# Kernel optimization log

Measured on AMD Instinct MI355X. Metric: run time of the kernel, lower is better.

## Reference

```python
import jax, jax.numpy as jnp
import numpy as np

# ---- static config (mirrors TALoss(num_classes=80, reg_max=16, strides=[8,16,32])) ----
B, M, NC, REG_MAX = 32, 20, 80, 16
STRIDES = (8, 16, 32)
HW = ((80, 80), (40, 40), (20, 20))          # feature map sizes for 640x640 input
NO = REG_MAX * 4 + NC                         # 144 channels per head
A = sum(h * w for h, w in HW)                 # 8400 anchors
TOPK, ALPHA, BETA = 10, 0.5, 6.0
BOX_G, CLS_G, DFL_G = 7.5, 0.5, 1.5
EPS = 1e-9


def setup_inputs() -> dict:
    key = jax.random.key(0)
    ks = jax.random.split(key, 6)
    feats = {f"feat{i}": jax.random.normal(ks[i], (B, NO, h, w), jnp.float32)
             for i, (h, w) in enumerate(HW)}
    # targets: (N,6) rows of (img_idx, class, cx, cy, w, h), normalized, 20 boxes/image, sorted by image
    img_idx = jnp.repeat(jnp.arange(B, dtype=jnp.float32), M)
    cls = jax.random.randint(ks[3], (B * M,), 0, NC).astype(jnp.float32)
    cxy = jax.random.uniform(ks[4], (B * M, 2), minval=0.2, maxval=0.8)
    wh = jax.random.uniform(ks[5], (B * M, 2), minval=0.05, maxval=0.3)
    targets = jnp.concatenate([img_idx[:, None], cls[:, None], cxy, wh], axis=1)
    return {**feats, "targets": targets}


def _make_anchors():
    pts, strs = [], []
    for (h, w), s in zip(HW, STRIDES):
        sx = jnp.arange(w, dtype=jnp.float32) + 0.5
        sy = jnp.arange(h, dtype=jnp.float32) + 0.5
        gy, gx = jnp.meshgrid(sy, sx, indexing="ij")
        pts.append(jnp.stack([gx, gy], -1).reshape(-1, 2))
        strs.append(jnp.full((h * w, 1), float(s), jnp.float32))
    return jnp.concatenate(pts), jnp.concatenate(strs)   # (A,2), (A,1)


def _ciou(b1, b2, eps=1e-7):
    # b1, b2: broadcastable xyxy boxes (..., 4) -> CIoU (...,)
    b1x1, b1y1, b1x2, b1y2 = b1[..., 0], b1[..., 1], b1[..., 2], b1[..., 3]
    b2x1, b2y1, b2x2, b2y2 = b2[..., 0], b2[..., 1], b2[..., 2], b2[..., 3]
    w1, h1 = b1x2 - b1x1, b1y2 - b1y1 + eps
    w2, h2 = b2x2 - b2x1, b2y2 - b2y1 + eps
    inter = (jnp.clip(jnp.minimum(b1x2, b2x2) - jnp.maximum(b1x1, b2x1), 0)
             * jnp.clip(jnp.minimum(b1y2, b2y2) - jnp.maximum(b1y1, b2y1), 0))
    union = w1 * h1 + w2 * h2 - inter + eps
    iou = inter / union
    cw = jnp.maximum(b1x2, b2x2) - jnp.minimum(b1x1, b2x1)
    ch = jnp.maximum(b1y2, b2y2) - jnp.minimum(b1y1, b2y1)
    c2 = cw ** 2 + ch ** 2 + eps
    rho2 = ((b2x1 + b2x2 - b1x1 - b1x2) ** 2 + (b2y1 + b2y2 - b1y1 - b1y2) ** 2) / 4.0
    v = (4.0 / np.pi ** 2) * (jnp.arctan(w2 / h2) - jnp.arctan(w1 / h1)) ** 2
    a = jax.lax.stop_gradient(v / (v - iou + (1.0 + eps)))   # torch: computed under no_grad
    return iou - (rho2 / c2 + v * a)


def _assign(pd_scores, pd_bboxes, anc, gt_labels, gt_bboxes, mask_gt):
    """TaskAlignedAssigner. pd_scores (B,A,NC) sigmoid-ed, pd_bboxes (B,A,4) image units,
    anc (A,2) image units, gt_labels (B,M), gt_bboxes (B,M,4), mask_gt (B,M) float."""
    # anchors inside each gt box -> (B,M,A)
    lt = anc[None, None, :, :] - gt_bboxes[:, :, None, :2]
    rb = gt_bboxes[:, :, None, 2:] - anc[None, None, :, :]
    mask_in = (jnp.concatenate([lt, rb], -1).min(-1) > EPS).astype(jnp.float32)
    mask = mask_in * mask_gt[..., None]                      # (B,M,A) candidate mask
    overlaps = jnp.clip(_ciou(gt_bboxes[:, :, None, :], pd_bboxes[:, None, :, :]), 0) * mask
    labels = gt_labels.astype(jnp.int32)                     # (B,M)
    # scores of each gt's class at every anchor: (B,M,A)
    bbox_scores = jnp.take_along_axis(pd_scores.transpose(0, 2, 1),
                                      jnp.broadcast_to(labels[:, :, None], (B, M, A)), axis=1) * mask
    align = (bbox_scores ** ALPHA) * (overlaps ** BETA)      # (B,M,A), already zero off-mask
    # top-k anchors per gt
    _, idxs = jax.lax.top_k(align, TOPK)                     # (B,M,K)
    idxs = jnp.where(mask_gt[..., None] > 0, idxs, 0)
    cnt = jax.nn.one_hot(idxs, A, dtype=jnp.float32).sum(-2)  # (B,M,A)
    mask_topk = jnp.where(cnt > 1, 0.0, cnt)
    mask_pos = mask_topk * mask
    # resolve anchors matched to multiple gts: keep the max-overlap gt
    fg = mask_pos.sum(1)                                     # (B,A)
    is_max = jnp.moveaxis(jax.nn.one_hot(overlaps.argmax(1), M, dtype=jnp.float32), -1, 1)  # (B,M,A)
    mask_pos = jnp.where(fg[:, None, :] > 1, is_max, mask_pos)
    fg = mask_pos.sum(1)
    tgt_idx = mask_pos.argmax(1)                             # (B,A)
    t_labels = jnp.take_along_axis(labels, tgt_idx, 1)       # (B,A)
    t_bboxes = jnp.take_along_axis(gt_bboxes, tgt_idx[..., None], 1)  # (B,A,4)
    fg_b = (fg > 0).astype(jnp.float32)
    t_scores = jax.nn.one_hot(t_labels, NC, dtype=jnp.float32) * fg_b[..., None]
    # normalize scores: align * (max overlap per gt) / (max align per gt)
    align_pos = align * mask_pos
    pos_align = align_pos.max(-1, keepdims=True)             # (B,M,1)
    pos_over = (overlaps * mask_pos).max(-1, keepdims=True)
    norm = (align_pos * pos_over / (pos_align + EPS)).max(1)  # (B,A)
    return t_bboxes, t_scores * norm[..., None], fg_b


def _forward(feat0, feat1, feat2, targets):
    feats = [feat0, feat1, feat2]
    pred = jnp.concatenate([f.reshape(B, NO, -1) for f in feats], axis=2)
    pred_distri = pred[:, :REG_MAX * 4].transpose(0, 2, 1)   # (B,A,64)
    pred_scores = pred[:, REG_MAX * 4:].transpose(0, 2, 1)   # (B,A,NC)
    anc, stride_t = _make_anchors()
    img_h, img_w = HW[0][0] * STRIDES[0], HW[0][1] * STRIDES[0]
    scale = jnp.array([img_w, img_h, img_w, img_h], jnp.float32)
    # ---- preprocess targets (N,6) -> padded (B,M,5), xywh*scale -> xyxy ----
    idx = targets[:, 0].astype(jnp.int32)
    pos = jnp.arange(targets.shape[0]) - jnp.searchsorted(idx, idx, side="left")
    out = jnp.zeros((B, M, 5), jnp.float32).at[idx, pos].set(targets[:, 1:])
    gt_labels = out[..., 0]
    xywh = out[..., 1:5] * scale
    gt_bboxes = jnp.concatenate([xywh[..., :2] - xywh[..., 2:] / 2,
                                 xywh[..., :2] + xywh[..., 2:] / 2], -1)
    mask_gt = (gt_bboxes.sum(-1) > 0).astype(jnp.float32)    # (B,M)
    # ---- DFL bbox decode (feature-map units) ----
    proj = jnp.arange(REG_MAX, dtype=jnp.float32)
    dist = jax.nn.softmax(pred_distri.reshape(B, A, 4, REG_MAX), -1) @ proj  # (B,A,4) ltrb
    pred_bboxes = jnp.concatenate([anc - dist[..., :2], anc + dist[..., 2:]], -1)
    # ---- task-aligned assignment (on detached preds, image units) ----
    pd_scores = jax.lax.stop_gradient(jax.nn.sigmoid(pred_scores))
    pd_bboxes = jax.lax.stop_gradient(pred_bboxes) * stride_t
    target_bboxes, target_scores, fg_mask = _assign(pd_scores, pd_bboxes, anc * stride_t,
                                                    gt_labels, gt_bboxes, mask_gt)
    target_bboxes = target_bboxes / stride_t
    tss = jnp.maximum(target_scores.sum(), 1.0)
    # ---- BCE-with-logits classification loss (pos_weight=1) ----
    x, t = pred_scores, target_scores
    bce = jnp.maximum(x, 0) - x * t + jnp.log1p(jnp.exp(-jnp.abs(x)))
    loss_cls = bce.sum() / tss
    # ---- CIoU box loss + DFL, weighted by per-anchor target score sum on fg ----
    weight = target_scores.sum(-1) * fg_mask                 # (B,A)
    iou = _ciou(pred_bboxes, target_bboxes)
    loss_box = ((1.0 - iou) * weight).sum() / tss
    tltrb = jnp.clip(jnp.concatenate([anc - target_bboxes[..., :2],
                                      target_bboxes[..., 2:] - anc], -1),
                     0, REG_MAX - 1 - 0.01)                  # (B,A,4)
    logp = jax.nn.log_softmax(pred_distri.reshape(B, A, 4, REG_MAX), -1)
    tl = tltrb.astype(jnp.int32)
    wl = (tl + 1).astype(jnp.float32) - tltrb
    nll_l = -jnp.take_along_axis(logp, tl[..., None], -1)[..., 0]
    nll_r = -jnp.take_along_axis(logp, (tl + 1)[..., None], -1)[..., 0]
    dfl = (nll_l * wl + nll_r * (1.0 - wl)).mean(-1)         # (B,A)
    loss_dfl = (dfl * weight).sum() / tss
    losses = jnp.stack([loss_box * BOX_G, loss_cls * CLS_G, loss_dfl * DFL_G])
    return losses.sum() * B, jax.lax.stop_gradient(losses)


def reference(feat0, feat1, feat2, targets):
    return _forward(feat0, feat1, feat2, targets)
```

## Files before the change

kernel.cpp:

```cpp
#include <hip/hip_runtime.h>
#include <math.h>

constexpr int BB  = 32;
constexpr int MM  = 20;
constexpr int NCC = 80;
constexpr int RM  = 16;
constexpr int NOC = 144;
constexpr int AT  = 8400;
constexpr int TK  = 10;
constexpr int BA  = BB * AT;
constexpr int BM  = BB * MM;
constexpr int MAXPOS = BM * TK;
constexpr int NSLOT = 1024;
constexpr float EPS_A = 1e-9f;
constexpr float VCOEF = 0.40528473456935108577551785283891f;

constexpr int NBOX0 = BB * 6400 / 256;
constexpr int NBOX1 = BB * 1600 / 256;
constexpr int NBOX2 = BB * 400 / 256;
constexpr int NBOX  = NBOX0 + NBOX1 + NBOX2;

struct Lvl { const float* f; int o, w, hw; float s; };

__device__ inline Lvl level_of(int a, const float* f0, const float* f1, const float* f2){
  Lvl L;
  if (a < 6400)      { L.f = f0; L.o = a;        L.w = 80; L.hw = 6400; L.s = 8.f;  }
  else if (a < 8000) { L.f = f1; L.o = a - 6400; L.w = 40; L.hw = 1600; L.s = 16.f; }
  else               { L.f = f2; L.o = a - 8000; L.w = 20; L.hw = 400;  L.s = 32.f; }
  return L;
}

__device__ inline float frcp(float x){ return __builtin_amdgcn_rcpf(x); }

__device__ inline float fast_atan(float x){
  float ax = fabsf(x);
  bool big = ax > 1.f;
  float z = big ? frcp(ax) : ax;
  float z2 = z * z;
  float p = fmaf(z2, -0.0117212f, 0.0526533f);
  p = fmaf(z2, p, -0.1164329f);
  p = fmaf(z2, p, 0.1935435f);
  p = fmaf(z2, p, -0.3326235f);
  p = fmaf(z2, p, 0.9999773f);
  float r = z * p;
  r = big ? 1.57079632679f - r : r;
  return copysignf(r, x);
}

__device__ inline float ciou_f(float b1x1,float b1y1,float b1x2,float b1y2,
                               float b2x1,float b2y1,float b2x2,float b2y2){
  const float eps = 1e-7f;
  float w1 = b1x2 - b1x1, h1 = b1y2 - b1y1 + eps;
  float w2 = b2x2 - b2x1, h2 = b2y2 - b2y1 + eps;
  float iw = fmaxf(fminf(b1x2, b2x2) - fmaxf(b1x1, b2x1), 0.f);
  float ih = fmaxf(fminf(b1y2, b2y2) - fmaxf(b1y1, b2y1), 0.f);
  float inter = iw * ih;
  float uni = w1 * h1 + w2 * h2 - inter + eps;
  float iou = inter * frcp(uni);
  float cw = fmaxf(b1x2, b2x2) - fminf(b1x1, b2x1);
  float ch = fmaxf(b1y2, b2y2) - fminf(b1y1, b2y1);
  float c2 = cw * cw + ch * ch + eps;
  float dx = b2x1 + b2x2 - b1x1 - b1x2;
  float dy = b2y1 + b2y2 - b1y1 - b1y2;
  float rho2 = (dx * dx + dy * dy) * 0.25f;
  float r1 = w1 * frcp(h1), r2 = w2 * frcp(h2);
  float dat = fast_atan((r2 - r1) * frcp(fmaf(r1, r2, 1.f)));
  float v = VCOEF * dat * dat;
  float alpha = v * frcp(v - iou + (1.0f + eps));
  return iou - (rho2 * frcp(c2) + v * alpha);
}

__device__ inline unsigned long long shfl_xor_u64(unsigned long long v, int mask){
  int lo = __shfl_xor((int)(unsigned)(v & 0xFFFFFFFFull), mask);
  int hi = __shfl_xor((int)(unsigned)(v >> 32), mask);
  return ((unsigned long long)(unsigned)hi << 32) | (unsigned)lo;
}

__device__ inline float softplus1(float x){
  return fmaxf(x, 0.f) + __logf(1.f + __expf(-fabsf(x)));
}

template<int HW, int W, int AOFF>
__device__ inline float fused_tile(const float* __restrict__ f, int u,
                                   float4* __restrict__ pbox,
                                   float4* __restrict__ lseg,
                                   unsigned* __restrict__ mpos){
  int b = u / HW, o = u - b * HW;
  const float* base = f + (size_t)b * NOC * HW + o;

  float d[4], ls[4];
#pragma unroll
  for (int side = 0; side < 4; side++){
    float x[16];
#pragma unroll
    for (int j = 0; j < 16; j++)
      x[j] = base[(size_t)((side * 16 + j) * HW)];
    float mx = x[0];
#pragma unroll
    for (int j = 1; j < 16; j++) mx = fmaxf(mx, x[j]);
    float sm = 0.f, dt = 0.f;
#pragma unroll
    for (int j = 0; j < 16; j++){
      float e = __expf(x[j] - mx);
      sm += e; dt = fmaf(e, (float)j, dt);
    }
    d[side]  = dt * frcp(sm);
    ls[side] = mx + __logf(sm);
  }
  int iy = o / W;
  float ax = (float)(o - iy * W) + 0.5f;
  float ay = (float)iy + 0.5f;
  int gi = b * AT + AOFF + o;
  pbox[gi] = make_float4(ax - d[0], ay - d[1], ax + d[2], ay + d[3]);
  lseg[gi] = make_float4(ls[0], ls[1], ls[2], ls[3]);
  mpos[gi] = 0u;

  const float* cbase = base + (size_t)(4 * RM) * HW;
  float sp = 0.f;
#pragma unroll
  for (int jj = 0; jj < NCC; jj += 8){
    float x[8];
#pragma unroll
    for (int j = 0; j < 8; j++)
      x[j] = cbase[(size_t)((jj + j) * HW)];
#pragma unroll
    for (int j = 0; j < 8; j++)
      sp += softplus1(x[j]);
  }
  return sp;
}

__global__ __launch_bounds__(256, 4) void k_feat3(
    const float* __restrict__ f0, const float* __restrict__ f1,
    const float* __restrict__ f2, const float* __restrict__ tgt,
    float4* __restrict__ pbox, float4* __restrict__ lse,
    unsigned* __restrict__ mpos, double* __restrict__ bce_part,
    float* __restrict__ out5, float* __restrict__ gtbox,
    int* __restrict__ gtlab, float* __restrict__ gtmask,
    int* __restrict__ pa_i, int* __restrict__ po_i,
    int* __restrict__ topk_arr, double* __restrict__ acc){
  __shared__ float red[4];
  int blk = blockIdx.x;
  int tid = threadIdx.x;
  if (blk < NBOX){
    float sp;
    if (blk < NBOX0){
      sp = fused_tile<6400, 80, 0>(f0, blk * 256 + tid, pbox, lse, mpos);
    } else if (blk < NBOX0 + NBOX1){
      sp = fused_tile<1600, 40, 6400>(f1, (blk - NBOX0) * 256 + tid, pbox, lse, mpos);
    } else {
      sp = fused_tile<400, 20, 8000>(f2, (blk - NBOX0 - NBOX1) * 256 + tid, pbox, lse, mpos);
    }
    for (int off = 32; off; off >>= 1) sp += __shfl_down(sp, off);
    int wid = tid >> 6, lid = tid & 63;
    if (lid == 0) red[wid] = sp;
    __syncthreads();
    if (tid == 0) bce_part[blk] = (double)(red[0] + red[1] + red[2] + red[3]);
  } else {
    for (int i = tid; i < BM * 5; i += 256) out5[i] = 0.f;
    for (int i = tid; i < MAXPOS; i += 256) topk_arr[i] = -1;
    for (int i = tid; i < BM; i += 256){ pa_i[i] = 0; po_i[i] = 0; }
    if (tid < 8) acc[tid] = 0.0;
    __syncthreads();
    for (int t = tid; t < BM; t += 256){
      int img = (int)tgt[t * 6 + 0];
      int j = t;
      while (j > 0 && (int)tgt[(j - 1) * 6 + 0] == img) j--;
      int pos = t - j;
      if (img >= 0 && img < BB && pos < MM){
        for (int k = 0; k < 5; k++)
          out5[(img * MM + pos) * 5 + k] = tgt[t * 6 + 1 + k];
      }
    }
    __syncthreads();
    for (int t = tid; t < BM; t += 256){
      float lab = out5[t * 5 + 0];
      float cx = out5[t * 5 + 1] * 640.f;
      float cy = out5[t * 5 + 2] * 640.f;
      float w  = out5[t * 5 + 3] * 640.f;
      float h  = out5[t * 5 + 4] * 640.f;
      float x1 = cx - w * 0.5f, y1 = cy - h * 0.5f;
      float x2 = cx + w * 0.5f, y2 = cy + h * 0.5f;
      gtbox[t * 4 + 0] = x1; gtbox[t * 4 + 1] = y1;
      gtbox[t * 4 + 2] = x2; gtbox[t * 4 + 3] = y2;
      gtlab[t] = (int)lab;
      gtmask[t] = ((x1 + y1 + x2 + y2) > 0.f) ? 1.f : 0.f;
    }
  }
}

__global__ __launch_bounds__(256) void k_align(
    const float* __restrict__ f0, const float* __restrict__ f1,
    const float* __restrict__ f2, const float4* __restrict__ pbox,
    const float* __restrict__ gtbox, const int* __restrict__ gtlab,
    const float* __restrict__ gtmask,
    unsigned* __restrict__ mpos, int* __restrict__ topk_arr){
  int pair = blockIdx.x;
  int b = pair / MM, m = pair % MM;
  if (gtmask[pair] <= 0.f) return;
  int tid = threadIdx.x;
  float gx1 = gtbox[pair * 4 + 0], gy1 = gtbox[pair * 4 + 1];
  float gx2 = gtbox[pair * 4 + 2], gy2 = gtbox[pair * 4 + 3];
  int lab = gtlab[pair];
  __shared__ float s_val[NSLOT];
  __shared__ int   s_anc[NSLOT];
  __shared__ unsigned long long s_red[4];
  __shared__ int   s_win[TK];
  int base = 0;

#define PROC_LEVEL(FPTR, W, HW, AOFF, S)                                      \
  {                                                                           \
    const float s_ = (S); const float inv_ = 1.f / (S);                       \
    int x0 = max(0, (int)floorf(gx1 * inv_ - 0.5f));                          \
    int x1 = min((W) - 1, (int)ceilf(gx2 * inv_ - 0.5f));                     \
    int y0 = max(0, (int)floorf(gy1 * inv_ - 0.5f));                          \
    int y1 = min((W) - 1, (int)ceilf(gy2 * inv_ - 0.5f));                     \
    int nxx = x1 - x0 + 1, nyy = y1 - y0 + 1;                                 \
    if (nxx > 0 && nyy > 0){                                                  \
      int ntot = nxx * nyy;                                                   \
      unsigned magic = 0xFFFFFFFFu / (unsigned)nxx + 1u;                      \
      const float* clsrow = (FPTR) + (size_t)b * NOC * (HW)                   \
                            + (size_t)(4 * RM + lab) * (HW);                  \
      for (int t = tid; t < ntot; t += 256){                                  \
        int slot = base + t;                                                  \
        if (slot >= NSLOT) break;                                             \
        int iy = (int)(((unsigned long long)(unsigned)t * magic) >> 32);      \
        int ix = t - iy * nxx + x0;                                           \
        iy += y0;                                                             \
        float ax = ((float)ix + 0.5f) * s_;                                   \
        float ay = ((float)iy + 0.5f) * s_;                                   \
        float mn = fminf(fminf(ax - gx1, ay - gy1),                           \
                         fminf(gx2 - ax, gy2 - ay));                          \
        int o = iy * (W) + ix;                                                \
        int a = (AOFF) + o;                                                   \
        float aln = -1.f;                                                     \
        if (mn > EPS_A){                                                      \
          float4 pb = pbox[b * AT + a];                                       \
          float c = ciou_f(gx1, gy1, gx2, gy2,                                \
                           pb.x * s_, pb.y * s_, pb.z * s_, pb.w * s_);       \
          float ovl = fmaxf(c, 0.f);                                          \
          if (ovl > 0.f){                                                     \
            float xv = clsrow[o];                                             \
            float sc = frcp(1.f + __expf(-xv));                               \
            float o2 = ovl * ovl;                                             \
            aln = sqrtf(sc) * (o2 * o2 * o2);                                 \
          }                                                                   \
        }                                                                     \
        s_val[slot] = aln;                                                    \
        s_anc[slot] = a;                                                      \
      }                                                                       \
      base += ntot;                                                           \
    }                                                                         \
  }

  PROC_LEVEL(f0, 80, 6400, 0, 8.f)
  PROC_LEVEL(f1, 40, 1600, 6400, 16.f)
  PROC_LEVEL(f2, 20, 400, 8000, 32.f)
#undef PROC_LEVEL

  __syncthreads();
  int total = min(base, NSLOT);
  int wid = tid >> 6, lid = tid & 63;
  for (int r = 0; r < TK; r++){
    unsigned long long key = 0ULL;
    for (int i = tid; i < total; i += 256){
      float v = s_val[i];
      if (v > 0.f){
        unsigned long long k2 =
            ((unsigned long long)__float_as_uint(v) << 32) |
            (unsigned long long)(0xFFFFFFFFu - (unsigned)i);
        key = key > k2 ? key : k2;
      }
    }
    for (int xm = 1; xm < 64; xm <<= 1){
      unsigned long long o = shfl_xor_u64(key, xm);
      key = key > o ? key : o;
    }
    if (lid == 0) s_red[wid] = key;
    __syncthreads();
    if (tid == 0){
      unsigned long long k = s_red[0];
      k = k > s_red[1] ? k : s_red[1];
      k = k > s_red[2] ? k : s_red[2];
      k = k > s_red[3] ? k : s_red[3];
      if (k){
        int slot = (int)(0xFFFFFFFFu - (unsigned)(k & 0xFFFFFFFFull));
        s_win[r] = s_anc[slot];
        s_val[slot] = -1.f;
      } else s_win[r] = -1;
    }
    __syncthreads();
  }
  if (tid < TK){
    int a = s_win[tid];
    topk_arr[pair * TK + tid] = a;
    if (a >= 0) atomicOr(&mpos[(size_t)b * AT + a], 1u << m);
  }
}

__global__ __launch_bounds__(256) void k_resolve(
    const float* __restrict__ f0, const float* __restrict__ f1,
    const float* __restrict__ f2, const float4* __restrict__ pbox,
    const float* __restrict__ gtbox, const int* __restrict__ gtlab,
    const float* __restrict__ gtmask, const unsigned* __restrict__ mpos,
    const int* __restrict__ topk_arr,
    unsigned char* __restrict__ resm, float* __restrict__ resaln,
    int* __restrict__ pa_i, int* __restrict__ po_i){
  int i = blockIdx.x * 256 + threadIdx.x;
  int a = topk_arr[i];
  if (a < 0) return;
  int pair = i / TK;
  int b = pair / MM, m = pair % MM;
  unsigned bits = mpos[(size_t)b * AT + a];
  if (m != __ffs(bits) - 1) return;
  Lvl L = level_of(a, f0, f1, f2);
  float ax = ((float)(L.o % L.w) + 0.5f) * L.s;
  float ay = ((float)(L.o / L.w) + 0.5f) * L.s;
  float4 pb = pbox[b * AT + a];
  float px1 = pb.x * L.s, py1 = pb.y * L.s, px2 = pb.z * L.s, py2 = pb.w * L.s;
  int mr; float ovl;
  if (__popc(bits) > 1){
    float best = -1.f; int bm = 0;
    for (int mm = 0; mm < MM; mm++){
      float v = 0.f;
      if (gtmask[b * MM + mm] > 0.f){
        float x1 = gtbox[(b * MM + mm) * 4 + 0], y1 = gtbox[(b * MM + mm) * 4 + 1];
        float x2 = gtbox[(b * MM + mm) * 4 + 2], y2 = gtbox[(b * MM + mm) * 4 + 3];
        float mn = fminf(fminf(ax - x1, ay - y1), fminf(x2 - ax, y2 - ay));
        if (mn > EPS_A)
          v = fmaxf(ciou_f(x1, y1, x2, y2, px1, py1, px2, py2), 0.f);
      }
      if (v > best){ best = v; bm = mm; }
    }
    mr = bm; ovl = fmaxf(best, 0.f);
  } else {
    mr = m;
    float x1 = gtbox[(b * MM + mr) * 4 + 0], y1 = gtbox[(b * MM + mr) * 4 + 1];
    float x2 = gtbox[(b * MM + mr) * 4 + 2], y2 = gtbox[(b * MM + mr) * 4 + 3];
    ovl = fmaxf(ciou_f(x1, y1, x2, y2, px1, py1, px2, py2), 0.f);
  }
  int lab = gtlab[b * MM + mr];
  float xv = L.f[(size_t)b * NOC * L.hw + (size_t)(4 * RM + lab) * L.hw + L.o];
  float sc = frcp(1.f + __expf(-xv));
  float o2 = ovl * ovl;
  float aln = sqrtf(sc) * (o2 * o2 * o2);
  size_t gi = (size_t)b * AT + a;
  resm[gi] = (unsigned char)mr;
  resaln[gi] = aln;
  atomicMax(&pa_i[b * MM + mr], __float_as_int(aln));
  atomicMax(&po_i[b * MM + mr], __float_as_int(ovl));
}

__global__ __launch_bounds__(256) void k_final(
    const float* __restrict__ f0, const float* __restrict__ f1,
    const float* __restrict__ f2,
    const float4* __restrict__ pbox, const float4* __restrict__ lse,
    const float* __restrict__ gtbox, const int* __restrict__ gtlab,
    const int* __restrict__ pa_i, const int* __restrict__ po_i,
    const unsigned* __restrict__ mpos, const int* __restrict__ topk_arr,
    const unsigned char* __restrict__ resm, const float* __restrict__ resaln,
    double* __restrict__ acc){
  int i = blockIdx.x * 256 + threadIdx.x;
  float w_ = 0.f, clsp = 0.f, boxp = 0.f, dflp = 0.f;
  int a = topk_arr[i];
  if (a >= 0){
    int pair = i / TK;
    int b = pair / MM, m = pair % MM;
    unsigned bits = mpos[(size_t)b * AT + a];
    if (m == __ffs(bits) - 1){
      size_t gi = (size_t)b * AT + a;
      int mr = (int)resm[gi];
      float aln = resaln[gi];
      float pa = __int_as_float(pa_i[b * MM + mr]);
      float po = __int_as_float(po_i[b * MM + mr]);
      w_ = aln * po * frcp(pa + EPS_A);
      Lvl L = level_of(a, f0, f1, f2);
      const float* base = L.f + (size_t)b * NOC * L.hw + L.o;
      float ax = (float)(L.o % L.w) + 0.5f;
      float ay = (float)(L.o / L.w) + 0.5f;
      float inv_s = frcp(L.s);
      float tx1 = gtbox[(b * MM + mr) * 4 + 0] * inv_s, ty1 = gtbox[(b * MM + mr) * 4 + 1] * inv_s;
      float tx2 = gtbox[(b * MM + mr) * 4 + 2] * inv_s, ty2 = gtbox[(b * MM + mr) * 4 + 3] * inv_s;
      float4 pb = pbox[b * AT + a];
      float iou = ciou_f(pb.x, pb.y, pb.z, pb.w, tx1, ty1, tx2, ty2);
      boxp = (1.f - iou) * w_;
      float4 L4 = lse[b * AT + a];
      float lsv[4] = { L4.x, L4.y, L4.z, L4.w };
      float tv[4] = { ax - tx1, ay - ty1, tx2 - ax, ty2 - ay };
      float dfl = 0.f;
#pragma unroll
      for (int s4 = 0; s4 < 4; s4++){
        float t = fminf(fmaxf(tv[s4], 0.f), (float)(RM - 1) - 0.01f);
        int tl = (int)t;
        float wl = (float)(tl + 1) - t;
        float xl = base[(size_t)(s4 * RM + tl) * L.hw];
        float xr = base[(size_t)(s4 * RM + tl + 1) * L.hw];
        dfl += (lsv[s4] - xl) * wl + (lsv[s4] - xr) * (1.f - wl);
      }
      dflp = dfl * 0.25f * w_;
      int lab = gtlab[b * MM + mr];
      clsp = base[(size_t)(4 * RM + lab) * L.hw] * w_;
    }
  }
  __shared__ float red[4][4];
  float vals[4] = { w_, clsp, boxp, dflp };
  int wid = threadIdx.x >> 6, lid = threadIdx.x & 63;
#pragma unroll
  for (int j = 0; j < 4; j++){
    float v = vals[j];
    for (int off = 32; off; off >>= 1) v += __shfl_down(v, off);
    if (lid == 0) red[wid][j] = v;
  }
  __syncthreads();
  if (threadIdx.x == 0){
    float t0 = 0.f, t1 = 0.f, t2 = 0.f, t3 = 0.f;
    for (int w2 = 0; w2 < 4; w2++){
      t0 += red[w2][0]; t1 += red[w2][1]; t2 += red[w2][2]; t3 += red[w2][3];
    }
    atomicAdd(&acc[0], (double)t0);
    atomicAdd(&acc[1], (double)t1);
    atomicAdd(&acc[2], (double)t2);
    atomicAdd(&acc[3], (double)t3);
  }
}

__global__ void k_out(const double* __restrict__ acc,
                      const double* __restrict__ bce_part,
                      float* __restrict__ out){
  __shared__ double sd[256];
  double s = 0.0;
  for (int i = threadIdx.x; i < NBOX; i += 256) s += bce_part[i];
  sd[threadIdx.x] = s;
  __syncthreads();
  for (int off = 128; off; off >>= 1){
    if (threadIdx.x < off) sd[threadIdx.x] += sd[threadIdx.x + off];
    __syncthreads();
  }
  if (threadIdx.x == 0){
    double bce_sum = sd[0];
    double tss = acc[0] > 1.0 ? acc[0] : 1.0;
    double loss_box = acc[2] / tss;
    double loss_cls = (bce_sum - acc[1]) / tss;
    double loss_dfl = acc[3] / tss;
    float l0 = (float)(loss_box * 7.5);
    float l1 = (float)(loss_cls * 0.5);
    float l2 = (float)(loss_dfl * 1.5);
    out[0] = (l0 + l1 + l2) * 32.f;
    out[1] = l0;
    out[2] = l1;
    out[3] = l2;
  }
}

extern "C" void kernel_launch(void* const* d_in, const int* in_sizes, int n_in,
                              void* d_out, int out_size, void* d_ws, size_t ws_size,
                              hipStream_t stream) {
  const float* f0 = (const float*)d_in[0];
  const float* f1 = (const float*)d_in[1];
  const float* f2 = (const float*)d_in[2];
  const float* tg = (const float*)d_in[3];
  float* out = (float*)d_out;

  char* w = (char*)d_ws;
  size_t off = 0;
  auto alloc = [&](size_t bytes) -> void* {
    void* p = w + off;
    off += (bytes + 255) & ~(size_t)255;
    return p;
  };
  float4*        pbox    = (float4*)       alloc((size_t)BA * 16);
  float4*        lse     = (float4*)       alloc((size_t)BA * 16);
  float*         gtbox   = (float*)        alloc((size_t)BM * 16);
  int*           gtlab   = (int*)          alloc((size_t)BM * 4);
  float*         gtmask  = (float*)        alloc((size_t)BM * 4);
  float*         out5    = (float*)        alloc((size_t)BM * 20);
  unsigned*      mpos    = (unsigned*)     alloc((size_t)BA * 4);
  int*           topk_arr= (int*)          alloc((size_t)MAXPOS * 4);
  unsigned char* resm    = (unsigned char*)alloc((size_t)BA);
  float*         resaln  = (float*)        alloc((size_t)BA * 4);
  int*           pa      = (int*)          alloc((size_t)BM * 4);
  int*           po      = (int*)          alloc((size_t)BM * 4);
  double*        acc     = (double*)       alloc(8 * 8);
  double*        bcep    = (double*)       alloc((size_t)NBOX * 8);

  k_feat3<<<NBOX + 1, 256, 0, stream>>>(f0, f1, f2, tg, pbox, lse, mpos, bcep,
                                        out5, gtbox, gtlab, gtmask, pa, po,
                                        topk_arr, acc);
  k_align<<<BM, 256, 0, stream>>>(f0, f1, f2, pbox, gtbox, gtlab, gtmask, mpos, topk_arr);
  k_resolve<<<MAXPOS / 256, 256, 0, stream>>>(f0, f1, f2, pbox, gtbox, gtlab, gtmask,
                                              mpos, topk_arr, resm, resaln, pa, po);
  k_final<<<MAXPOS / 256, 256, 0, stream>>>(f0, f1, f2, pbox, lse, gtbox, gtlab,
                                            pa, po, mpos, topk_arr, resm, resaln, acc);
  k_out<<<1, 256, 0, stream>>>(acc, bcep, out);
}
```

Before: 249.7 us.

## Stage DFL channels through LDS with float4 loads and vectorize class softplus

The feature kernel is restructured into per-image tiles of up to 256 anchors. Each tile loads the 64 distribution channels with coalesced float4 loads into a 64KB shared buffer, then one thread per anchor computes the softmax from shared memory. The class-channel softplus sum now also reads float4 vectors. This targets the cost of scalar strided global loads, but the 64KB LDS per block limits occupancy and partial tiles leave threads idle.

Result: no change. 248.5 us (-0.5%).

```diff
diff --git a/kernel.cpp b/kernel.cpp
--- a/kernel.cpp
+++ b/kernel.cpp
@@ -15,10 +15,8 @@
 constexpr float EPS_A = 1e-9f;
 constexpr float VCOEF = 0.40528473456935108577551785283891f;
 
-constexpr int NBOX0 = BB * 6400 / 256;
-constexpr int NBOX1 = BB * 1600 / 256;
-constexpr int NBOX2 = BB * 400 / 256;
-constexpr int NBOX  = NBOX0 + NBOX1 + NBOX2;
+constexpr int TPI    = 34;
+constexpr int NTILES = BB * TPI;
 
 struct Lvl { const float* f; int o, w, hw; float s; };
 
@@ -76,61 +74,93 @@
   return ((unsigned long long)(unsigned)hi << 32) | (unsigned)lo;
 }
 
-__device__ inline float softplus1(float x){
-  return fmaxf(x, 0.f) + __logf(1.f + __expf(-fabsf(x)));
-}
-
-template<int HW, int W, int AOFF>
-__device__ inline float fused_tile(const float* __restrict__ f, int u,
-                                   float4* __restrict__ pbox,
-                                   float4* __restrict__ lseg,
-                                   unsigned* __restrict__ mpos){
-  int b = u / HW, o = u - b * HW;
-  const float* base = f + (size_t)b * NOC * HW + o;
-
-  float d[4], ls[4];
-#pragma unroll
-  for (int side = 0; side < 4; side++){
-    float x[16];
-#pragma unroll
-    for (int j = 0; j < 16; j++)
-      x[j] = base[(size_t)((side * 16 + j) * HW)];
-    float mx = x[0];
-#pragma unroll
-    for (int j = 1; j < 16; j++) mx = fmaxf(mx, x[j]);
-    float sm = 0.f, dt = 0.f;
-#pragma unroll
-    for (int j = 0; j < 16; j++){
-      float e = __expf(x[j] - mx);
-      sm += e; dt = fmaf(e, (float)j, dt);
-    }
-    d[side]  = dt * frcp(sm);
-    ls[side] = mx + __logf(sm);
-  }
-  int iy = o / W;
-  float ax = (float)(o - iy * W) + 0.5f;
-  float ay = (float)iy + 0.5f;
-  int gi = b * AT + AOFF + o;
-  pbox[gi] = make_float4(ax - d[0], ay - d[1], ax + d[2], ay + d[3]);
-  lseg[gi] = make_float4(ls[0], ls[1], ls[2], ls[3]);
-  mpos[gi] = 0u;
+__device__ inline float softplus4(float4 v){
+  float s = fmaxf(v.x, 0.f) + __logf(1.f + __expf(-fabsf(v.x)));
+  s += fmaxf(v.y, 0.f) + __logf(1.f + __expf(-fabsf(v.y)));
+  s += fmaxf(v.z, 0.f) + __logf(1.f + __expf(-fabsf(v.z)));
+  s += fmaxf(v.w, 0.f) + __logf(1.f + __expf(-fabsf(v.w)));
+  return s;
+}
+
+template<int NA, int HW, int W, int AOFF>
+__device__ inline float feat_tile(const float* __restrict__ f, int b, int o0,
+                                  float* __restrict__ sT,
+                                  float4* __restrict__ pbox,
+                                  float4* __restrict__ lse,
+                                  unsigned* __restrict__ mpos){
+  constexpr int NA4  = NA / 4;
+  constexpr int NDF4 = 64 * NA4;
+  constexpr int NIT  = NDF4 / 256;
+  int tid = threadIdx.x;
+  const float* base = f + (size_t)b * NOC * HW + o0;
+
+  {
+    float4 x[NIT];
+#pragma unroll
+    for (int k = 0; k < NIT; k++){
+      int idx = k * 256 + tid;
+      int ch = idx / NA4, pos = idx - ch * NA4;
+      x[k] = *(const float4*)(base + (size_t)ch * HW + pos * 4);
+    }
+#pragma unroll
+    for (int k = 0; k < NIT; k++){
+      int idx = k * 256 + tid;
+      int ch = idx / NA4, pos = idx - ch * NA4;
+      *(float4*)(&sT[ch * NA + pos * 4]) = x[k];
+    }
+  }
+  __syncthreads();
+
+  if (tid < NA){
+    float d[4], ls[4];
+#pragma unroll
+    for (int s = 0; s < 4; s++){
+      float xs[16];
+#pragma unroll
+      for (int j = 0; j < 16; j++) xs[j] = sT[(s * 16 + j) * NA + tid];
+      float mx = xs[0];
+#pragma unroll
+      for (int j = 1; j < 16; j++) mx = fmaxf(mx, xs[j]);
+      float sm = 0.f, dt = 0.f;
+#pragma unroll
+      for (int j = 0; j < 16; j++){
+        float e = __expf(xs[j] - mx);
+        sm += e; dt = fmaf(e, (float)j, dt);
+      }
+      d[s]  = dt * frcp(sm);
+      ls[s] = mx + __logf(sm);
+    }
+    int o = o0 + tid;
+    int iy = o / W;
+    float ax = (float)(o - iy * W) + 0.5f;
+    float ay = (float)iy + 0.5f;
+    int gi = b * AT + AOFF + o;
+    pbox[gi] = make_float4(ax - d[0], ay - d[1], ax + d[2], ay + d[3]);
+    lse[gi]  = make_float4(ls[0], ls[1], ls[2], ls[3]);
+    mpos[gi] = 0u;
+  }
 
   const float* cbase = base + (size_t)(4 * RM) * HW;
+  constexpr int NCF4 = 80 * NA4;
+  constexpr int NKC  = NCF4 / 256;
   float sp = 0.f;
 #pragma unroll
-  for (int jj = 0; jj < NCC; jj += 8){
-    float x[8];
-#pragma unroll
-    for (int j = 0; j < 8; j++)
-      x[j] = cbase[(size_t)((jj + j) * HW)];
-#pragma unroll
-    for (int j = 0; j < 8; j++)
-      sp += softplus1(x[j]);
+  for (int k = 0; k < NKC; k++){
+    int idx = k * 256 + tid;
+    int ch = idx / NA4, pos = idx - ch * NA4;
+    sp += softplus4(*(const float4*)(cbase + (size_t)ch * HW + pos * 4));
+  }
+  if constexpr (NCF4 % 256 != 0){
+    int idx = NKC * 256 + tid;
+    if (idx < NCF4){
+      int ch = idx / NA4, pos = idx - ch * NA4;
+      sp += softplus4(*(const float4*)(cbase + (size_t)ch * HW + pos * 4));
+    }
   }
   return sp;
 }
 
-__global__ __launch_bounds__(256, 4) void k_feat3(
+__global__ __launch_bounds__(256) void k_feat6(
     const float* __restrict__ f0, const float* __restrict__ f1,
     const float* __restrict__ f2, const float* __restrict__ tgt,
     float4* __restrict__ pbox, float4* __restrict__ lse,
@@ -139,18 +169,18 @@
     int* __restrict__ gtlab, float* __restrict__ gtmask,
     int* __restrict__ pa_i, int* __restrict__ po_i,
     int* __restrict__ topk_arr, double* __restrict__ acc){
+  __shared__ float sT[64 * 256];
   __shared__ float red[4];
   int blk = blockIdx.x;
   int tid = threadIdx.x;
-  if (blk < NBOX){
+  if (blk < NTILES){
+    int b = blk / TPI, tt = blk - b * TPI;
     float sp;
-    if (blk < NBOX0){
-      sp = fused_tile<6400, 80, 0>(f0, blk * 256 + tid, pbox, lse, mpos);
-    } else if (blk < NBOX0 + NBOX1){
-      sp = fused_tile<1600, 40, 6400>(f1, (blk - NBOX0) * 256 + tid, pbox, lse, mpos);
-    } else {
-      sp = fused_tile<400, 20, 8000>(f2, (blk - NBOX0 - NBOX1) * 256 + tid, pbox, lse, mpos);
-    }
+    if (tt < 25)       sp = feat_tile<256, 6400, 80, 0>   (f0, b, tt * 256,        sT, pbox, lse, mpos);
+    else if (tt < 31)  sp = feat_tile<256, 1600, 40, 6400>(f1, b, (tt - 25) * 256, sT, pbox, lse, mpos);
+    else if (tt == 31) sp = feat_tile< 64, 1600, 40, 6400>(f1, b, 1536,            sT, pbox, lse, mpos);
+    else if (tt == 32) sp = feat_tile<256,  400, 20, 8000>(f2, b, 0,               sT, pbox, lse, mpos);
+    else               sp = feat_tile<144,  400, 20, 8000>(f2, b, 256,             sT, pbox, lse, mpos);
     for (int off = 32; off; off >>= 1) sp += __shfl_down(sp, off);
     int wid = tid >> 6, lid = tid & 63;
     if (lid == 0) red[wid] = sp;
@@ -429,7 +459,7 @@
                       float* __restrict__ out){
   __shared__ double sd[256];
   double s = 0.0;
-  for (int i = threadIdx.x; i < NBOX; i += 256) s += bce_part[i];
+  for (int i = threadIdx.x; i < NTILES; i += 256) s += bce_part[i];
   sd[threadIdx.x] = s;
   __syncthreads();
   for (int off = 128; off; off >>= 1){
@@ -481,11 +511,11 @@
   int*           pa      = (int*)          alloc((size_t)BM * 4);
   int*           po      = (int*)          alloc((size_t)BM * 4);
   double*        acc     = (double*)       alloc(8 * 8);
-  double*        bcep    = (double*)       alloc((size_t)NBOX * 8);
-
-  k_feat3<<<NBOX + 1, 256, 0, stream>>>(f0, f1, f2, tg, pbox, lse, mpos, bcep,
-                                        out5, gtbox, gtlab, gtmask, pa, po,
-                                        topk_arr, acc);
+  double*        bcep    = (double*)       alloc((size_t)NTILES * 8);
+
+  k_feat6<<<NTILES + 1, 256, 0, stream>>>(f0, f1, f2, tg, pbox, lse, mpos, bcep,
+                                          out5, gtbox, gtlab, gtmask, pa, po,
+                                          topk_arr, acc);
   k_align<<<BM, 256, 0, stream>>>(f0, f1, f2, pbox, gtbox, gtlab, gtmask, mpos, topk_arr);
   k_resolve<<<MAXPOS / 256, 256, 0, stream>>>(f0, f1, f2, pbox, gtbox, gtlab, gtmask,
                                               mpos, topk_arr, resm, resaln, pa, po);
```
